# Optimization experiments

Measured on AMD Instinct MI355X. Metric: run time of the kernel, lower is better.

Reference implementation:

```python
import jax, jax.numpy as jnp
import numpy as np

N, E, D_IN, D_OUT = 50000, 800000, 128, 128
LN_EPS = 1e-5


def setup_inputs() -> dict:
    key = jax.random.key(0)
    ks = jax.random.split(key, 7)
    x = jax.random.normal(ks[0], (N, D_IN), dtype=jnp.float32)
    adj = jax.random.randint(ks[1], (2, E), 0, N, dtype=jnp.int32)  # edge_index
    scale = 1.0 / np.sqrt(D_IN)
    W_gcn = jax.random.normal(ks[2], (D_IN, D_OUT), dtype=jnp.float32) * scale
    b_gcn = jax.random.normal(ks[3], (D_OUT,), dtype=jnp.float32) * 0.02
    W_lin = jax.random.normal(ks[4], (D_IN, D_OUT), dtype=jnp.float32) * scale
    ln_w = jnp.ones((D_OUT,), dtype=jnp.float32)
    ln_b = jnp.zeros((D_OUT,), dtype=jnp.float32)
    return {"adj": adj, "x": x, "W_gcn": W_gcn, "b_gcn": b_gcn,
            "W_lin": W_lin, "ln_w": ln_w, "ln_b": ln_b}


def _gcn_conv(x, edge_index, W, b):
    """PyG GCNConv: add self-loops, symmetric D^-1/2 (A+I) D^-1/2 normalization."""
    n = x.shape[0]
    loop = jnp.arange(n, dtype=edge_index.dtype)
    src = jnp.concatenate([edge_index[0], loop])  # message sources (x_j)
    dst = jnp.concatenate([edge_index[1], loop])  # aggregation targets
    ones = jnp.ones(src.shape[0], dtype=x.dtype)
    deg = jax.ops.segment_sum(ones, dst, num_segments=n)
    dinv = jnp.where(deg > 0, jax.lax.rsqrt(deg), 0.0)
    norm = dinv[src] * dinv[dst]                   # [E+N]
    h = x @ W                                      # [N, D_OUT] project first (PyG order)
    msg = h[src] * norm[:, None]                   # gather + scale
    agg = jax.ops.segment_sum(msg, dst, num_segments=n)
    return agg + b


def _layer_norm(y, w, b):
    mu = jnp.mean(y, axis=-1, keepdims=True)
    var = jnp.mean(jnp.square(y - mu), axis=-1, keepdims=True)
    return (y - mu) * jax.lax.rsqrt(var + LN_EPS) * w + b


def reference(adj, x, W_gcn, b_gcn, W_lin, ln_w, ln_b):
    x1 = _gcn_conv(x, adj, W_gcn, b_gcn)
    x2 = x @ W_lin                                  # bias=False linear
    return _layer_norm(x1 + x2 + 1e-6, ln_w, ln_b)
```

## Files before the change

kernel.cpp:

```cpp
#include <hip/hip_runtime.h>
#include <hip/hip_bf16.h>

#define NN 50000
#define EE 800000
#define DD 128
#define CB 196
#define NFB 1563
#define EBLK 2048
#define NEB 391

typedef __attribute__((ext_vector_type(8))) short bf16x8;
typedef __attribute__((ext_vector_type(4))) float f32x4;

static __device__ __forceinline__ unsigned short f2bf(float f) {
  union { float f; unsigned u; } v; v.f = f;
  unsigned r = v.u + 0x7FFFu + ((v.u >> 16) & 1u);
  return (unsigned short)(r >> 16);
}
static __device__ __forceinline__ float bf2f(unsigned short h) {
  union { unsigned u; float f; } v; v.u = ((unsigned)h) << 16;
  return v.f;
}

__global__ __launch_bounds__(256) void k_p0(
    const int* __restrict__ dst, int* __restrict__ coarseCnt,
    const float* __restrict__ Wg, const float* __restrict__ Wl,
    unsigned short* __restrict__ Wt, const float4* __restrict__ x4,
    ushort4* __restrict__ xb4) {
  int b = blockIdx.x, t = threadIdx.x;
  if (b < NEB) {
    __shared__ int cnt[CB];
    for (int i = t; i < CB; i += 256) cnt[i] = 0;
    __syncthreads();
    int e0 = b * EBLK;
    for (int i = t; i < EBLK; i += 256) {
      int e = e0 + i;
      if (e < EE) atomicAdd(&cnt[dst[e] >> 8], 1);
    }
    __syncthreads();
    for (int i = t; i < CB; i += 256)
      if (cnt[i]) atomicAdd(&coarseCnt[i], cnt[i]);
  } else if (b < NEB + 32) {
    for (int i = (b - NEB) * 256 + t; i < DD * 256; i += 32 * 256) {
      int n = i >> 8, k = i & 255;
      float v = (k < 128) ? Wg[k * DD + n] : Wl[(k - 128) * DD + n];
      Wt[i] = f2bf(v);
    }
  } else {
    int base = (b - NEB - 32) * 1024 + t;
#pragma unroll
    for (int k = 0; k < 4; k++) {
      int i = base + k * 256;
      if (i < NN * 32) {
        float4 v = x4[i];
        ushort4 o;
        o.x = f2bf(v.x); o.y = f2bf(v.y); o.z = f2bf(v.z); o.w = f2bf(v.w);
        xb4[i] = o;
      }
    }
  }
}

__global__ __launch_bounds__(256) void k_pscan(const int* __restrict__ coarseCnt,
                                               int* __restrict__ coarseStart,
                                               int* __restrict__ cursor) {
  __shared__ int s[256];
  int t = threadIdx.x;
  int v = (t < CB) ? coarseCnt[t] : 0;
  s[t] = v;
  for (int off = 1; off < 256; off <<= 1) {
    __syncthreads();
    int tmp = (t >= off) ? s[t - off] : 0;
    __syncthreads();
    if (t >= off) s[t] += tmp;
  }
  __syncthreads();
  if (t < CB) {
    coarseStart[t] = s[t] - v;
    cursor[t] = s[t] - v;
  }
}

__global__ __launch_bounds__(256) void k_p1a(const int* __restrict__ src,
                                             const int* __restrict__ dst,
                                             int* __restrict__ cursor,
                                             unsigned int* __restrict__ pairs) {
  __shared__ unsigned int stage[EBLK];
  __shared__ int cnt[CB], base_[CB], cur[CB];
  int t = threadIdx.x;
  int e0 = blockIdx.x * EBLK;
  for (int i = t; i < CB; i += 256) { cnt[i] = 0; cur[i] = 0; }
  __syncthreads();
  for (int i = t; i < EBLK; i += 256) {
    int e = e0 + i;
    unsigned int p = 0xFFFFFFFFu;
    if (e < EE) {
      int d = dst[e], s = src[e];
      int cb = d >> 8;
      p = (unsigned int)s | ((unsigned int)(d & 255) << 16) | ((unsigned int)cb << 24);
      atomicAdd(&cnt[cb], 1);
    }
    stage[i] = p;
  }
  __syncthreads();
  for (int i = t; i < CB; i += 256)
    base_[i] = cnt[i] ? atomicAdd(&cursor[i], cnt[i]) : 0;
  __syncthreads();
  for (int i = t; i < EBLK; i += 256) {
    unsigned int p = stage[i];
    if (p != 0xFFFFFFFFu) {
      int cb = p >> 24;
      int ofs = atomicAdd(&cur[cb], 1);
      pairs[base_[cb] + ofs] = p;
    }
  }
}

__global__ __launch_bounds__(512) void k_p1b(
    const unsigned int* __restrict__ pairs, const int* __restrict__ coarseStart,
    const int* __restrict__ coarseCnt, const unsigned short* __restrict__ xb,
    int* __restrict__ deg, float* __restrict__ dinv, int* __restrict__ rowStart,
    unsigned short* __restrict__ srcU16, unsigned short* __restrict__ xs) {
  __shared__ int ldeg[256], lscan[256], lcur[256];
  __shared__ float ldinvs[256];
  int cb = blockIdx.x, t = threadIdx.x;
  int start = coarseStart[cb], cnt = coarseCnt[cb];
  int n0 = cb << 8;
  int nloc = NN - n0; if (nloc > 256) nloc = 256;
  if (t < 256) ldeg[t] = 0;
  __syncthreads();
  for (int i = t; i < cnt; i += 512)
    atomicAdd(&ldeg[(pairs[start + i] >> 16) & 255], 1);
  __syncthreads();
  if (t < 256) lscan[t] = ldeg[t];
  for (int off = 1; off < 256; off <<= 1) {
    __syncthreads();
    int tmp = (t >= off && t < 256) ? lscan[t - off] : 0;
    __syncthreads();
    if (t >= off && t < 256) lscan[t] += tmp;
  }
  __syncthreads();
  if (t < 256) {
    int dg = ldeg[t];
    int rs = start + lscan[t] - dg;
    lcur[t] = rs;
    float di = rsqrtf((float)(dg + 1));
    ldinvs[t] = di;
    if (t < nloc) { deg[n0 + t] = dg; dinv[n0 + t] = di; rowStart[n0 + t] = rs; }
  }
  __syncthreads();
  for (int i = t; i < cnt; i += 512) {
    unsigned int pr = pairs[start + i];
    int pos = atomicAdd(&lcur[(pr >> 16) & 255], 1);
    srcU16[pos] = (unsigned short)(pr & 0xFFFFu);
  }
  for (int i = t; i < nloc * 16; i += 512) {
    int rr = i >> 4, q = i & 15;
    bf16x8 v = *(const bf16x8*)(xb + (size_t)(n0 + rr) * DD + q * 8);
    float di = ldinvs[rr];
    bf16x8 o;
#pragma unroll
    for (int k = 0; k < 8; k++) o[k] = (short)f2bf(bf2f((unsigned short)v[k]) * di);
    *(bf16x8*)(xs + (size_t)(n0 + rr) * DD + q * 8) = o;
  }
}

static __device__ __forceinline__ void gather16(
    const unsigned short* __restrict__ xs, const unsigned short* __restrict__ srcU16,
    int js, int cnt, int r, int srcLaneBase, float* acc) {
  for (int base = 0; base < cnt; base += 16) {
    int idx = (base + r < cnt) ? (int)srcU16[js + base + r] : 0;
    int m = cnt - base; if (m > 16) m = 16;
    int j = 0;
    for (; j + 4 <= m; j += 4) {
      int s0 = __shfl(idx, srcLaneBase + j);
      int s1 = __shfl(idx, srcLaneBase + j + 1);
      int s2 = __shfl(idx, srcLaneBase + j + 2);
      int s3 = __shfl(idx, srcLaneBase + j + 3);
      bf16x8 v0 = *(const bf16x8*)(xs + (size_t)s0 * DD + r * 8);
      bf16x8 v1 = *(const bf16x8*)(xs + (size_t)s1 * DD + r * 8);
      bf16x8 v2 = *(const bf16x8*)(xs + (size_t)s2 * DD + r * 8);
      bf16x8 v3 = *(const bf16x8*)(xs + (size_t)s3 * DD + r * 8);
#pragma unroll
      for (int k = 0; k < 8; k++) acc[k] += bf2f((unsigned short)v0[k]);
#pragma unroll
      for (int k = 0; k < 8; k++) acc[k] += bf2f((unsigned short)v1[k]);
#pragma unroll
      for (int k = 0; k < 8; k++) acc[k] += bf2f((unsigned short)v2[k]);
#pragma unroll
      for (int k = 0; k < 8; k++) acc[k] += bf2f((unsigned short)v3[k]);
    }
    for (; j < m; j++) {
      int s = __shfl(idx, srcLaneBase + j);
      bf16x8 v = *(const bf16x8*)(xs + (size_t)s * DD + r * 8);
#pragma unroll
      for (int k = 0; k < 8; k++) acc[k] += bf2f((unsigned short)v[k]);
    }
  }
}

__global__ __launch_bounds__(256) void k_mega3(
    const unsigned short* __restrict__ xs, const unsigned short* __restrict__ xb,
    const int* __restrict__ rowStart, const int* __restrict__ deg,
    const unsigned short* __restrict__ srcU16, const float* __restrict__ dinv,
    const unsigned short* __restrict__ Wt, const float* __restrict__ bgcn,
    const float* __restrict__ lnw, const float* __restrict__ lnb,
    float* __restrict__ out) {
  __shared__ unsigned short abuf[32 * 136];
  int b = blockIdx.x, t = threadIdx.x;
  int n0 = b * 32;
  int g = t >> 4, r = t & 15;
  int lane = t & 63;
  int srcLaneBase = lane & 48;
  int nA = n0 + g;
  int nB = n0 + g + 16;
  bool vB = (nB < NN);
  float acc0[8], acc1[8];
  {
    bf16x8 va = *(const bf16x8*)(xs + (size_t)nA * DD + r * 8);
#pragma unroll
    for (int k = 0; k < 8; k++) acc0[k] = bf2f((unsigned short)va[k]);
    if (vB) {
      bf16x8 vb = *(const bf16x8*)(xs + (size_t)nB * DD + r * 8);
#pragma unroll
      for (int k = 0; k < 8; k++) acc1[k] = bf2f((unsigned short)vb[k]);
    } else {
#pragma unroll
      for (int k = 0; k < 8; k++) acc1[k] = 0.f;
    }
  }
  gather16(xs, srcU16, rowStart[nA], deg[nA], r, srcLaneBase, acc0);
  if (vB) gather16(xs, srcU16, rowStart[nB], deg[nB], r, srcLaneBase, acc1);
  {
    float dA = dinv[nA];
    bf16x8 oa, ob;
#pragma unroll
    for (int k = 0; k < 8; k++) oa[k] = (short)f2bf(acc0[k] * dA);
    if (vB) {
      float dB = dinv[nB];
#pragma unroll
      for (int k = 0; k < 8; k++) ob[k] = (short)f2bf(acc1[k] * dB);
    } else {
#pragma unroll
      for (int k = 0; k < 8; k++) ob[k] = 0;
    }
    *(bf16x8*)&abuf[g * 136 + r * 8] = oa;
    *(bf16x8*)&abuf[(g + 16) * 136 + r * 8] = ob;
  }
  __syncthreads();
  if (t < 128) {
    int w = t >> 6, lane2 = t & 63;
    int quad = lane2 >> 4, rr = lane2 & 15;
    int mloc = w * 16 + rr;
    int rowA = n0 + mloc; int rc = (rowA < NN) ? rowA : (NN - 1);
    f32x4 zero = {0.f, 0.f, 0.f, 0.f};
    f32x4 macc[8];
#pragma unroll
    for (int i = 0; i < 8; i++) macc[i] = zero;
#pragma unroll
    for (int ks = 0; ks < 8; ks++) {
      bf16x8 a;
      if (ks < 4) a = *(const bf16x8*)&abuf[mloc * 136 + ks * 32 + quad * 8];
      else        a = *(const bf16x8*)(xb + (size_t)rc * DD + (ks - 4) * 32 + quad * 8);
#pragma unroll
      for (int nt = 0; nt < 8; nt++) {
        bf16x8 bb = *(const bf16x8*)(Wt + (size_t)(nt * 16 + rr) * 256 + ks * 32 + quad * 8);
        macc[nt] = __builtin_amdgcn_mfma_f32_16x16x32_bf16(a, bb, macc[nt], 0, 0, 0);
      }
    }
    float bg[8], lw[8], lb[8];
#pragma unroll
    for (int nt = 0; nt < 8; nt++) {
      int col = nt * 16 + rr;
      bg[nt] = bgcn[col] + 1e-6f;
      lw[nt] = lnw[col];
      lb[nt] = lnb[col];
    }
#pragma unroll
    for (int reg = 0; reg < 4; reg++) {
      float y[8];
      float s1 = 0.f, s2 = 0.f;
#pragma unroll
      for (int nt = 0; nt < 8; nt++) {
        y[nt] = macc[nt][reg] + bg[nt];
        s1 += y[nt];
        s2 += y[nt] * y[nt];
      }
#pragma unroll
      for (int off = 1; off < 16; off <<= 1) {
        s1 += __shfl_xor(s1, off);
        s2 += __shfl_xor(s2, off);
      }
      float mu = s1 * (1.0f / 128.0f);
      float var = s2 * (1.0f / 128.0f) - mu * mu;
      float inv = rsqrtf(var + 1e-5f);
      int row = n0 + w * 16 + quad * 4 + reg;
      if (row < NN) {
#pragma unroll
        for (int nt = 0; nt < 8; nt++) {
          out[(size_t)row * DD + nt * 16 + rr] = (y[nt] - mu) * inv * lw[nt] + lb[nt];
        }
      }
    }
  }
}

extern "C" void kernel_launch(void* const* d_in, const int* in_sizes, int n_in,
                              void* d_out, int out_size, void* d_ws, size_t ws_size,
                              hipStream_t stream) {
  const int* adj = (const int*)d_in[0];
  const float* x = (const float*)d_in[1];
  const float* Wg = (const float*)d_in[2];
  const float* bg = (const float*)d_in[3];
  const float* Wl = (const float*)d_in[4];
  const float* lw = (const float*)d_in[5];
  const float* lb = (const float*)d_in[6];
  const int* srcp = adj;
  const int* dstp = adj + EE;
  float* out = (float*)d_out;

  char* ws = (char*)d_ws;
  size_t off = 0;
  auto alloc = [&](size_t bytes) -> void* {
    void* p = ws + off;
    off += (bytes + 255) & ~(size_t)255;
    return p;
  };
  int* coarseCnt = (int*)alloc((size_t)CB * 4);
  int* coarseStart = (int*)alloc((size_t)CB * 4);
  int* cursor = (int*)alloc((size_t)CB * 4);
  unsigned int* pairs = (unsigned int*)alloc((size_t)EE * 4);
  unsigned short* srcU16 = (unsigned short*)alloc((size_t)EE * 2);
  int* deg = (int*)alloc((size_t)NN * 4);
  float* dinv = (float*)alloc((size_t)NN * 4);
  int* rowStart = (int*)alloc((size_t)NN * 4);
  unsigned short* xb = (unsigned short*)alloc((size_t)NN * DD * 2);
  unsigned short* xs = (unsigned short*)alloc((size_t)NN * DD * 2);
  unsigned short* Wt = (unsigned short*)alloc((size_t)DD * 256 * 2);
  (void)ws_size; (void)in_sizes; (void)n_in; (void)out_size;

  hipMemsetAsync(coarseCnt, 0, (size_t)CB * 4, stream);
  k_p0<<<NEB + 32 + 1563, 256, 0, stream>>>(dstp, coarseCnt, Wg, Wl, Wt,
                                            (const float4*)x, (ushort4*)xb);
  k_pscan<<<1, 256, 0, stream>>>(coarseCnt, coarseStart, cursor);
  k_p1a<<<NEB, 256, 0, stream>>>(srcp, dstp, cursor, pairs);
  k_p1b<<<CB, 512, 0, stream>>>(pairs, coarseStart, coarseCnt, xb, deg, dinv,
                                rowStart, srcU16, xs);
  k_mega3<<<NFB, 256, 0, stream>>>(xs, xb, rowStart, deg, srcU16, dinv, Wt,
                                   bg, lw, lb, out);
}
```

Before: 184.6 us.

## Split fused gather+MFMA kernel into separate aggregation and matmul-layernorm kernels

Replaces the fused kernel, in which half the threads idled during the MFMA/LayerNorm phase, with two kernels. The first is a pure gather-aggregation kernel that handles one node per 16 threads and unrolls the gather by 8 instead of 4. The second is an MFMA+LayerNorm kernel that uses all four waves per block. This should improve occupancy and memory-level parallelism in the gather. The cost is writing and re-reading a bf16 aggregate buffer through global memory, plus one extra launch.

```diff
diff --git a/kernel.cpp b/kernel.cpp
--- a/kernel.cpp
+++ b/kernel.cpp
@@ -5,7 +5,6 @@
 #define EE 800000
 #define DD 128
 #define CB 196
-#define NFB 1563
 #define EBLK 2048
 #define NEB 391
 
@@ -165,22 +164,43 @@
   }
 }
 
-static __device__ __forceinline__ void gather16(
-    const unsigned short* __restrict__ xs, const unsigned short* __restrict__ srcU16,
-    int js, int cnt, int r, int srcLaneBase, float* acc) {
+__global__ __launch_bounds__(256) void k_agg2(
+    const unsigned short* __restrict__ xs, const int* __restrict__ rowStart,
+    const int* __restrict__ deg, const unsigned short* __restrict__ srcU16,
+    const float* __restrict__ dinv, unsigned short* __restrict__ agg) {
+  int t = threadIdx.x;
+  int g = t >> 4, r = t & 15;
+  int node = blockIdx.x * 16 + g;
+  int lane = t & 63;
+  int srcLaneBase = lane & 48;
+  float acc[8];
+  {
+    bf16x8 vs = *(const bf16x8*)(xs + (size_t)node * DD + r * 8);
+#pragma unroll
+    for (int k = 0; k < 8; k++) acc[k] = bf2f((unsigned short)vs[k]);
+  }
+  int js = rowStart[node], cnt = deg[node];
   for (int base = 0; base < cnt; base += 16) {
     int idx = (base + r < cnt) ? (int)srcU16[js + base + r] : 0;
     int m = cnt - base; if (m > 16) m = 16;
     int j = 0;
-    for (; j + 4 <= m; j += 4) {
+    for (; j + 8 <= m; j += 8) {
       int s0 = __shfl(idx, srcLaneBase + j);
       int s1 = __shfl(idx, srcLaneBase + j + 1);
       int s2 = __shfl(idx, srcLaneBase + j + 2);
       int s3 = __shfl(idx, srcLaneBase + j + 3);
+      int s4 = __shfl(idx, srcLaneBase + j + 4);
+      int s5 = __shfl(idx, srcLaneBase + j + 5);
+      int s6 = __shfl(idx, srcLaneBase + j + 6);
+      int s7 = __shfl(idx, srcLaneBase + j + 7);
       bf16x8 v0 = *(const bf16x8*)(xs + (size_t)s0 * DD + r * 8);
       bf16x8 v1 = *(const bf16x8*)(xs + (size_t)s1 * DD + r * 8);
       bf16x8 v2 = *(const bf16x8*)(xs + (size_t)s2 * DD + r * 8);
       bf16x8 v3 = *(const bf16x8*)(xs + (size_t)s3 * DD + r * 8);
+      bf16x8 v4 = *(const bf16x8*)(xs + (size_t)s4 * DD + r * 8);
+      bf16x8 v5 = *(const bf16x8*)(xs + (size_t)s5 * DD + r * 8);
+      bf16x8 v6 = *(const bf16x8*)(xs + (size_t)s6 * DD + r * 8);
+      bf16x8 v7 = *(const bf16x8*)(xs + (size_t)s7 * DD + r * 8);
 #pragma unroll
       for (int k = 0; k < 8; k++) acc[k] += bf2f((unsigned short)v0[k]);
 #pragma unroll
@@ -189,6 +209,14 @@
       for (int k = 0; k < 8; k++) acc[k] += bf2f((unsigned short)v2[k]);
 #pragma unroll
       for (int k = 0; k < 8; k++) acc[k] += bf2f((unsigned short)v3[k]);
+#pragma unroll
+      for (int k = 0; k < 8; k++) acc[k] += bf2f((unsigned short)v4[k]);
+#pragma unroll
+      for (int k = 0; k < 8; k++) acc[k] += bf2f((unsigned short)v5[k]);
+#pragma unroll
+      for (int k = 0; k < 8; k++) acc[k] += bf2f((unsigned short)v6[k]);
+#pragma unroll
+      for (int k = 0; k < 8; k++) acc[k] += bf2f((unsigned short)v7[k]);
     }
     for (; j < m; j++) {
       int s = __shfl(idx, srcLaneBase + j);
@@ -197,109 +225,70 @@
       for (int k = 0; k < 8; k++) acc[k] += bf2f((unsigned short)v[k]);
     }
   }
-}
-
-__global__ __launch_bounds__(256) void k_mega3(
-    const unsigned short* __restrict__ xs, const unsigned short* __restrict__ xb,
-    const int* __restrict__ rowStart, const int* __restrict__ deg,
-    const unsigned short* __restrict__ srcU16, const float* __restrict__ dinv,
+  float d = dinv[node];
+  bf16x8 o;
+#pragma unroll
+  for (int k = 0; k < 8; k++) o[k] = (short)f2bf(acc[k] * d);
+  *(bf16x8*)(agg + (size_t)node * DD + r * 8) = o;
+}
+
+__global__ __launch_bounds__(256) void k_mm_ln(
+    const unsigned short* __restrict__ agg, const unsigned short* __restrict__ xb,
     const unsigned short* __restrict__ Wt, const float* __restrict__ bgcn,
     const float* __restrict__ lnw, const float* __restrict__ lnb,
     float* __restrict__ out) {
-  __shared__ unsigned short abuf[32 * 136];
-  int b = blockIdx.x, t = threadIdx.x;
-  int n0 = b * 32;
-  int g = t >> 4, r = t & 15;
-  int lane = t & 63;
-  int srcLaneBase = lane & 48;
-  int nA = n0 + g;
-  int nB = n0 + g + 16;
-  bool vB = (nB < NN);
-  float acc0[8], acc1[8];
-  {
-    bf16x8 va = *(const bf16x8*)(xs + (size_t)nA * DD + r * 8);
-#pragma unroll
-    for (int k = 0; k < 8; k++) acc0[k] = bf2f((unsigned short)va[k]);
-    if (vB) {
-      bf16x8 vb = *(const bf16x8*)(xs + (size_t)nB * DD + r * 8);
-#pragma unroll
-      for (int k = 0; k < 8; k++) acc1[k] = bf2f((unsigned short)vb[k]);
-    } else {
-#pragma unroll
-      for (int k = 0; k < 8; k++) acc1[k] = 0.f;
-    }
-  }
-  gather16(xs, srcU16, rowStart[nA], deg[nA], r, srcLaneBase, acc0);
-  if (vB) gather16(xs, srcU16, rowStart[nB], deg[nB], r, srcLaneBase, acc1);
-  {
-    float dA = dinv[nA];
-    bf16x8 oa, ob;
-#pragma unroll
-    for (int k = 0; k < 8; k++) oa[k] = (short)f2bf(acc0[k] * dA);
-    if (vB) {
-      float dB = dinv[nB];
-#pragma unroll
-      for (int k = 0; k < 8; k++) ob[k] = (short)f2bf(acc1[k] * dB);
-    } else {
-#pragma unroll
-      for (int k = 0; k < 8; k++) ob[k] = 0;
-    }
-    *(bf16x8*)&abuf[g * 136 + r * 8] = oa;
-    *(bf16x8*)&abuf[(g + 16) * 136 + r * 8] = ob;
-  }
-  __syncthreads();
-  if (t < 128) {
-    int w = t >> 6, lane2 = t & 63;
-    int quad = lane2 >> 4, rr = lane2 & 15;
-    int mloc = w * 16 + rr;
-    int rowA = n0 + mloc; int rc = (rowA < NN) ? rowA : (NN - 1);
-    f32x4 zero = {0.f, 0.f, 0.f, 0.f};
-    f32x4 macc[8];
-#pragma unroll
-    for (int i = 0; i < 8; i++) macc[i] = zero;
-#pragma unroll
-    for (int ks = 0; ks < 8; ks++) {
-      bf16x8 a;
-      if (ks < 4) a = *(const bf16x8*)&abuf[mloc * 136 + ks * 32 + quad * 8];
-      else        a = *(const bf16x8*)(xb + (size_t)rc * DD + (ks - 4) * 32 + quad * 8);
+  int t = threadIdx.x;
+  int w = t >> 6, lane = t & 63;
+  int quad = lane >> 4, r = lane & 15;
+  int m0 = (blockIdx.x * 4 + w) * 16;
+  f32x4 zero = {0.f, 0.f, 0.f, 0.f};
+  f32x4 acc[8];
+#pragma unroll
+  for (int i = 0; i < 8; i++) acc[i] = zero;
+  int rowA = m0 + r;
+  if (rowA > NN - 1) rowA = NN - 1;
+#pragma unroll
+  for (int ks = 0; ks < 8; ks++) {
+    bf16x8 a;
+    if (ks < 4) a = *(const bf16x8*)(agg + (size_t)rowA * DD + ks * 32 + quad * 8);
+    else        a = *(const bf16x8*)(xb + (size_t)rowA * DD + (ks - 4) * 32 + quad * 8);
+#pragma unroll
+    for (int nt = 0; nt < 8; nt++) {
+      bf16x8 b = *(const bf16x8*)(Wt + (size_t)(nt * 16 + r) * 256 + ks * 32 + quad * 8);
+      acc[nt] = __builtin_amdgcn_mfma_f32_16x16x32_bf16(a, b, acc[nt], 0, 0, 0);
+    }
+  }
+  float bg[8], lw[8], lb[8];
+#pragma unroll
+  for (int nt = 0; nt < 8; nt++) {
+    int col = nt * 16 + r;
+    bg[nt] = bgcn[col] + 1e-6f;
+    lw[nt] = lnw[col];
+    lb[nt] = lnb[col];
+  }
+#pragma unroll
+  for (int reg = 0; reg < 4; reg++) {
+    float y[8];
+    float s1 = 0.f, s2 = 0.f;
+#pragma unroll
+    for (int nt = 0; nt < 8; nt++) {
+      y[nt] = acc[nt][reg] + bg[nt];
+      s1 += y[nt];
+      s2 += y[nt] * y[nt];
+    }
+#pragma unroll
+    for (int off = 1; off < 16; off <<= 1) {
+      s1 += __shfl_xor(s1, off);
+      s2 += __shfl_xor(s2, off);
+    }
+    float mu = s1 * (1.0f / 128.0f);
+    float var = s2 * (1.0f / 128.0f) - mu * mu;
+    float inv = rsqrtf(var + 1e-5f);
+    int row = m0 + quad * 4 + reg;
+    if (row < NN) {
 #pragma unroll
       for (int nt = 0; nt < 8; nt++) {
-        bf16x8 bb = *(const bf16x8*)(Wt + (size_t)(nt * 16 + rr) * 256 + ks * 32 + quad * 8);
-        macc[nt] = __builtin_amdgcn_mfma_f32_16x16x32_bf16(a, bb, macc[nt], 0, 0, 0);
-      }
-    }
-    float bg[8], lw[8], lb[8];
-#pragma unroll
-    for (int nt = 0; nt < 8; nt++) {
-      int col = nt * 16 + rr;
-      bg[nt] = bgcn[col] + 1e-6f;
-      lw[nt] = lnw[col];
-      lb[nt] = lnb[col];
-    }
-#pragma unroll
-    for (int reg = 0; reg < 4; reg++) {
-      float y[8];
-      float s1 = 0.f, s2 = 0.f;
-#pragma unroll
-      for (int nt = 0; nt < 8; nt++) {
-        y[nt] = macc[nt][reg] + bg[nt];
-        s1 += y[nt];
-        s2 += y[nt] * y[nt];
-      }
-#pragma unroll
-      for (int off = 1; off < 16; off <<= 1) {
-        s1 += __shfl_xor(s1, off);
-        s2 += __shfl_xor(s2, off);
-      }
-      float mu = s1 * (1.0f / 128.0f);
-      float var = s2 * (1.0f / 128.0f) - mu * mu;
-      float inv = rsqrtf(var + 1e-5f);
-      int row = n0 + w * 16 + quad * 4 + reg;
-      if (row < NN) {
-#pragma unroll
-        for (int nt = 0; nt < 8; nt++) {
-          out[(size_t)row * DD + nt * 16 + rr] = (y[nt] - mu) * inv * lw[nt] + lb[nt];
-        }
+        out[(size_t)row * DD + nt * 16 + r] = (y[nt] - mu) * inv * lw[nt] + lb[nt];
       }
     }
   }
@@ -336,6 +325,7 @@
   int* rowStart = (int*)alloc((size_t)NN * 4);
   unsigned short* xb = (unsigned short*)alloc((size_t)NN * DD * 2);
   unsigned short* xs = (unsigned short*)alloc((size_t)NN * DD * 2);
+  unsigned short* agg = (unsigned short*)alloc((size_t)NN * DD * 2);
   unsigned short* Wt = (unsigned short*)alloc((size_t)DD * 256 * 2);
   (void)ws_size; (void)in_sizes; (void)n_in; (void)out_size;
 
@@ -346,6 +336,6 @@
   k_p1a<<<NEB, 256, 0, stream>>>(srcp, dstp, cursor, pairs);
   k_p1b<<<CB, 512, 0, stream>>>(pairs, coarseStart, coarseCnt, xb, deg, dinv,
                                 rowStart, srcU16, xs);
-  k_mega3<<<NFB, 256, 0, stream>>>(xs, xb, rowStart, deg, srcU16, dinv, Wt,
-                                   bg, lw, lb, out);
-}
+  k_agg2<<<3125, 256, 0, stream>>>(xs, rowStart, deg, srcU16, dinv, agg);
+  k_mm_ln<<<782, 256, 0, stream>>>(agg, xb, Wt, bg, lw, lb, out);
+}
```

Result: slower. 198.8 us (+7.7%).

## Fold coarse prefix scan into bucketing kernels, drop scan launch, widen gather unroll

Applied to the files above, without the earlier changes.

Removes the single-block scan kernel. Each k_p1a block now recomputes the exclusive scan of coarse counts and adds it to a zero-based per-bucket cursor, and k_p1b derives each bucket's start by summing the preceding counts with a warp reduction. Edge blocks double in size (4096 edges, 512 threads), which halves the block count. The gather loop is unrolled to 8 outstanding row loads. Together these cut a launch and raise memory-level parallelism, at the cost of redundant scan work in every block and higher register pressure in the gather.

```diff
diff --git a/kernel.cpp b/kernel.cpp
--- a/kernel.cpp
+++ b/kernel.cpp
@@ -6,8 +6,8 @@
 #define DD 128
 #define CB 196
 #define NFB 1563
-#define EBLK 2048
-#define NEB 391
+#define EBLK 4096
+#define NEB 196
 
 typedef __attribute__((ext_vector_type(8))) short bf16x8;
 typedef __attribute__((ext_vector_type(4))) float f32x4;
@@ -61,37 +61,21 @@
   }
 }
 
-__global__ __launch_bounds__(256) void k_pscan(const int* __restrict__ coarseCnt,
-                                               int* __restrict__ coarseStart,
-                                               int* __restrict__ cursor) {
-  __shared__ int s[256];
-  int t = threadIdx.x;
-  int v = (t < CB) ? coarseCnt[t] : 0;
-  s[t] = v;
-  for (int off = 1; off < 256; off <<= 1) {
-    __syncthreads();
-    int tmp = (t >= off) ? s[t - off] : 0;
-    __syncthreads();
-    if (t >= off) s[t] += tmp;
-  }
-  __syncthreads();
-  if (t < CB) {
-    coarseStart[t] = s[t] - v;
-    cursor[t] = s[t] - v;
-  }
-}
-
-__global__ __launch_bounds__(256) void k_p1a(const int* __restrict__ src,
+__global__ __launch_bounds__(512) void k_p1a(const int* __restrict__ src,
                                              const int* __restrict__ dst,
-                                             int* __restrict__ cursor,
+                                             const int* __restrict__ coarseCnt,
+                                             int* __restrict__ cursor0,
                                              unsigned int* __restrict__ pairs) {
   __shared__ unsigned int stage[EBLK];
-  __shared__ int cnt[CB], base_[CB], cur[CB];
+  __shared__ int sc[256];
+  __shared__ int cnt[CB], rb[CB], cur[CB];
   int t = threadIdx.x;
   int e0 = blockIdx.x * EBLK;
-  for (int i = t; i < CB; i += 256) { cnt[i] = 0; cur[i] = 0; }
-  __syncthreads();
-  for (int i = t; i < EBLK; i += 256) {
+  int own = 0;
+  if (t < CB) { cnt[t] = 0; cur[t] = 0; }
+  if (t < 256) { own = (t < CB) ? coarseCnt[t] : 0; sc[t] = own; }
+  __syncthreads();
+  for (int i = t; i < EBLK; i += 512) {
     int e = e0 + i;
     unsigned int p = 0xFFFFFFFFu;
     if (e < EE) {
@@ -102,46 +86,62 @@
     }
     stage[i] = p;
   }
-  __syncthreads();
-  for (int i = t; i < CB; i += 256)
-    base_[i] = cnt[i] ? atomicAdd(&cursor[i], cnt[i]) : 0;
-  __syncthreads();
-  for (int i = t; i < EBLK; i += 256) {
+  for (int off = 1; off < 256; off <<= 1) {
+    __syncthreads();
+    int tmp = (t < 256 && t >= off) ? sc[t - off] : 0;
+    __syncthreads();
+    if (t < 256 && t >= off) sc[t] += tmp;
+  }
+  __syncthreads();
+  if (t < CB) {
+    int excl = sc[t] - own;
+    rb[t] = excl + (cnt[t] ? atomicAdd(&cursor0[t], cnt[t]) : 0);
+  }
+  __syncthreads();
+  for (int i = t; i < EBLK; i += 512) {
     unsigned int p = stage[i];
     if (p != 0xFFFFFFFFu) {
       int cb = p >> 24;
       int ofs = atomicAdd(&cur[cb], 1);
-      pairs[base_[cb] + ofs] = p;
+      pairs[rb[cb] + ofs] = p;
     }
   }
 }
 
 __global__ __launch_bounds__(512) void k_p1b(
-    const unsigned int* __restrict__ pairs, const int* __restrict__ coarseStart,
-    const int* __restrict__ coarseCnt, const unsigned short* __restrict__ xb,
+    const unsigned int* __restrict__ pairs, const int* __restrict__ coarseCnt,
+    const unsigned short* __restrict__ xb,
     int* __restrict__ deg, float* __restrict__ dinv, int* __restrict__ rowStart,
     unsigned short* __restrict__ srcU16, unsigned short* __restrict__ xs) {
   __shared__ int ldeg[256], lscan[256], lcur[256];
   __shared__ float ldinvs[256];
-  int cb = blockIdx.x, t = threadIdx.x;
-  int start = coarseStart[cb], cnt = coarseCnt[cb];
-  int n0 = cb << 8;
+  __shared__ int wsum[8];
+  int b = blockIdx.x, t = threadIdx.x;
+  int n0 = b << 8;
   int nloc = NN - n0; if (nloc > 256) nloc = 256;
+  int partial = 0;
+  for (int i = t; i < b; i += 512) partial += coarseCnt[i];
+#pragma unroll
+  for (int off = 32; off > 0; off >>= 1) partial += __shfl_xor(partial, off);
+  if ((t & 63) == 0) wsum[t >> 6] = partial;
   if (t < 256) ldeg[t] = 0;
   __syncthreads();
+  int start = wsum[0] + wsum[1] + wsum[2] + wsum[3] +
+              wsum[4] + wsum[5] + wsum[6] + wsum[7];
+  int cnt = coarseCnt[b];
   for (int i = t; i < cnt; i += 512)
     atomicAdd(&ldeg[(pairs[start + i] >> 16) & 255], 1);
   __syncthreads();
-  if (t < 256) lscan[t] = ldeg[t];
+  int dg = (t < 256) ? ldeg[t] : 0;
+  if (t < 256) lscan[t] = dg;
   for (int off = 1; off < 256; off <<= 1) {
     __syncthreads();
-    int tmp = (t >= off && t < 256) ? lscan[t - off] : 0;
-    __syncthreads();
-    if (t >= off && t < 256) lscan[t] += tmp;
+    int tmp = (t < 256 && t >= off) ? lscan[t - off] : 0;
+    __syncthreads();
+    if (t < 256 && t >= off) lscan[t] += tmp;
   }
   __syncthreads();
   if (t < 256) {
-    int dg = ldeg[t];
     int rs = start + lscan[t] - dg;
     lcur[t] = rs;
     float di = rsqrtf((float)(dg + 1));
@@ -172,15 +172,23 @@
     int idx = (base + r < cnt) ? (int)srcU16[js + base + r] : 0;
     int m = cnt - base; if (m > 16) m = 16;
     int j = 0;
-    for (; j + 4 <= m; j += 4) {
+    for (; j + 8 <= m; j += 8) {
       int s0 = __shfl(idx, srcLaneBase + j);
       int s1 = __shfl(idx, srcLaneBase + j + 1);
       int s2 = __shfl(idx, srcLaneBase + j + 2);
       int s3 = __shfl(idx, srcLaneBase + j + 3);
+      int s4 = __shfl(idx, srcLaneBase + j + 4);
+      int s5 = __shfl(idx, srcLaneBase + j + 5);
+      int s6 = __shfl(idx, srcLaneBase + j + 6);
+      int s7 = __shfl(idx, srcLaneBase + j + 7);
       bf16x8 v0 = *(const bf16x8*)(xs + (size_t)s0 * DD + r * 8);
       bf16x8 v1 = *(const bf16x8*)(xs + (size_t)s1 * DD + r * 8);
       bf16x8 v2 = *(const bf16x8*)(xs + (size_t)s2 * DD + r * 8);
       bf16x8 v3 = *(const bf16x8*)(xs + (size_t)s3 * DD + r * 8);
+      bf16x8 v4 = *(const bf16x8*)(xs + (size_t)s4 * DD + r * 8);
+      bf16x8 v5 = *(const bf16x8*)(xs + (size_t)s5 * DD + r * 8);
+      bf16x8 v6 = *(const bf16x8*)(xs + (size_t)s6 * DD + r * 8);
+      bf16x8 v7 = *(const bf16x8*)(xs + (size_t)s7 * DD + r * 8);
 #pragma unroll
       for (int k = 0; k < 8; k++) acc[k] += bf2f((unsigned short)v0[k]);
 #pragma unroll
@@ -189,6 +197,14 @@
       for (int k = 0; k < 8; k++) acc[k] += bf2f((unsigned short)v2[k]);
 #pragma unroll
       for (int k = 0; k < 8; k++) acc[k] += bf2f((unsigned short)v3[k]);
+#pragma unroll
+      for (int k = 0; k < 8; k++) acc[k] += bf2f((unsigned short)v4[k]);
+#pragma unroll
+      for (int k = 0; k < 8; k++) acc[k] += bf2f((unsigned short)v5[k]);
+#pragma unroll
+      for (int k = 0; k < 8; k++) acc[k] += bf2f((unsigned short)v6[k]);
+#pragma unroll
+      for (int k = 0; k < 8; k++) acc[k] += bf2f((unsigned short)v7[k]);
     }
     for (; j < m; j++) {
       int s = __shfl(idx, srcLaneBase + j);
@@ -326,9 +342,9 @@
     off += (bytes + 255) & ~(size_t)255;
     return p;
   };
-  int* coarseCnt = (int*)alloc((size_t)CB * 4);
-  int* coarseStart = (int*)alloc((size_t)CB * 4);
-  int* cursor = (int*)alloc((size_t)CB * 4);
+  int* zb = (int*)alloc((size_t)512 * 4);
+  int* coarseCnt = zb;
+  int* cursor0 = zb + 256;
   unsigned int* pairs = (unsigned int*)alloc((size_t)EE * 4);
   unsigned short* srcU16 = (unsigned short*)alloc((size_t)EE * 2);
   int* deg = (int*)alloc((size_t)NN * 4);
@@ -339,13 +355,12 @@
   unsigned short* Wt = (unsigned short*)alloc((size_t)DD * 256 * 2);
   (void)ws_size; (void)in_sizes; (void)n_in; (void)out_size;
 
-  hipMemsetAsync(coarseCnt, 0, (size_t)CB * 4, stream);
+  hipMemsetAsync(zb, 0, (size_t)512 * 4, stream);
   k_p0<<<NEB + 32 + 1563, 256, 0, stream>>>(dstp, coarseCnt, Wg, Wl, Wt,
                                             (const float4*)x, (ushort4*)xb);
-  k_pscan<<<1, 256, 0, stream>>>(coarseCnt, coarseStart, cursor);
-  k_p1a<<<NEB, 256, 0, stream>>>(srcp, dstp, cursor, pairs);
-  k_p1b<<<CB, 512, 0, stream>>>(pairs, coarseStart, coarseCnt, xb, deg, dinv,
-                                rowStart, srcU16, xs);
+  k_p1a<<<NEB, 512, 0, stream>>>(srcp, dstp, coarseCnt, cursor0, pairs);
+  k_p1b<<<CB, 512, 0, stream>>>(pairs, coarseCnt, xb, deg, dinv, rowStart,
+                                srcU16, xs);
   k_mega3<<<NFB, 256, 0, stream>>>(xs, xb, rowStart, deg, srcU16, dinv, Wt,
                                    bg, lw, lb, out);
 }
```

After: 190.1 us. 2.9% more time.
